# Performance work log

Measured on AMD Instinct MI355X. Metric: run time of the kernel, lower is better.

The kernel has to match this reference:

```python
import jax, jax.numpy as jnp
import numpy as np

B = 16384       # batch size
P = 2           # fixed pooling factor per bag (offsets are arange * P)
NTAB = 26       # number of sparse feature tables
NROWS = 100000  # rows per embedding table
D = 128         # embedding dim == ln_bot[-1]
LN_BOT = [13, 512, 256, 128]
LN_TOP = [479, 1024, 512, 256, 1]


def setup_inputs() -> dict:
    key = jax.random.key(0)
    ks = jax.random.split(key, 32)
    inp = {}
    inp['dense_x'] = jax.random.normal(ks[0], (B, LN_BOT[0]), dtype=jnp.float32)
    # offsets: uniform stride-P bags (EmbeddingBag offsets)
    inp['lS_o'] = jnp.broadcast_to(jnp.arange(B, dtype=jnp.int64) * P, (NTAB, B))
    inp['lS_i'] = jax.random.randint(ks[1], (NTAB, B * P), 0, NROWS, dtype=jnp.int64)
    # embedding tables, uniform(-sqrt(1/n), sqrt(1/n))
    bound = float(np.sqrt(1.0 / NROWS))
    inp['emb_tables'] = jax.random.uniform(ks[2], (NTAB, NROWS, D), dtype=jnp.float32,
                                           minval=-bound, maxval=bound)
    # bot MLP params (He-style scaled normal)
    ki = 3
    for i in range(len(LN_BOT) - 1):
        n, m = LN_BOT[i], LN_BOT[i + 1]
        inp[f'bw{i}'] = jax.random.normal(ks[ki], (m, n), dtype=jnp.float32) * np.sqrt(2.0 / (m + n)); ki += 1
        inp[f'bb{i}'] = jax.random.normal(ks[ki], (m,), dtype=jnp.float32) * np.sqrt(1.0 / m); ki += 1
    for i in range(len(LN_TOP) - 1):
        n, m = LN_TOP[i], LN_TOP[i + 1]
        inp[f'tw{i}'] = jax.random.normal(ks[ki], (m, n), dtype=jnp.float32) * np.sqrt(2.0 / (m + n)); ki += 1
        inp[f'tb{i}'] = jax.random.normal(ks[ki], (m,), dtype=jnp.float32) * np.sqrt(1.0 / m); ki += 1
    return inp


def _mlp(x, Ws, bs, sigmoid_layer):
    for i, (W, b) in enumerate(zip(Ws, bs)):
        x = x @ W.T + b
        x = jax.nn.sigmoid(x) if i == sigmoid_layer else jax.nn.relu(x)
    return x


def reference(dense_x, lS_o, lS_i, emb_tables,
              bw0, bb0, bw1, bb1, bw2, bb2,
              tw0, tb0, tw1, tb1, tw2, tb2, tw3, tb3):
    # bot MLP (sigmoid_bot = -1 -> all ReLU)
    x = _mlp(dense_x, [bw0, bw1, bw2], [bb0, bb1, bb2], sigmoid_layer=-1)  # [B, D]

    # multi-table EmbeddingBag sum pooling. Offsets (lS_o) are uniform stride-P
    # arange bags, so sum pooling is a gather + reshape + sum over P.
    def pool_one(table, idx):
        return table[idx].reshape(B, P, D).sum(axis=1)  # [B, D]
    ly = jax.vmap(pool_one)(emb_tables, lS_i)  # [NTAB, B, D]

    # dot interaction (arch_interaction_itself=False -> strict lower triangle)
    T = jnp.concatenate([x[:, None, :], jnp.transpose(ly, (1, 0, 2))], axis=1)  # [B, 27, D]
    Z = jnp.einsum('bid,bjd->bij', T, T)  # [B, 27, 27]
    ni = NTAB + 1
    li, lj = jnp.tril_indices(ni, k=-1)
    Zflat = Z[:, li, lj]  # [B, 351]
    R = jnp.concatenate([x, Zflat], axis=1)  # [B, 479]

    # top MLP (sigmoid at last layer, sigmoid_top = 3)
    p = _mlp(R, [tw0, tw1, tw2, tw3], [tb0, tb1, tb2, tb3], sigmoid_layer=3)
    return p  # [B, 1]
```

## Files before the change

### kernel.cpp

```cpp
#include <hip/hip_runtime.h>
#include <hip/hip_bf16.h>
#include <math.h>

#define BATCH 16384
#define NTAB 26
#define DIM 128
#define NROWS 100000

typedef short bf16x8 __attribute__((ext_vector_type(8)));
typedef float f32x4 __attribute__((ext_vector_type(4)));
typedef float f32x16 __attribute__((ext_vector_type(16)));

__device__ __forceinline__ ushort f2b(float f) {
  union { float f; unsigned u; } c; c.f = f;
  unsigned r = (c.u + 0x7fffu + ((c.u >> 16) & 1u)) >> 16;
  return (ushort)r;
}
__device__ __forceinline__ float b2f(ushort u) {
  union { unsigned u; float f; } c; c.u = (unsigned)u << 16;
  return c.f;
}

__device__ __forceinline__ void gload_lds16(const void* g, void* l) {
  __builtin_amdgcn_global_load_lds(
      (const __attribute__((address_space(1))) void*)g,
      (__attribute__((address_space(3))) void*)l, 16, 0, 0);
}

__global__ __launch_bounds__(256) void cvt_all_kernel(
    const float* __restrict__ bw1, const float* __restrict__ bw2,
    const float* __restrict__ tw0, const float* __restrict__ tw1,
    const float* __restrict__ tw2,
    ushort* __restrict__ o1, ushort* __restrict__ o2, ushort* __restrict__ o3,
    ushort* __restrict__ o4, ushort* __restrict__ o5) {
  int i = blockIdx.x * 256 + threadIdx.x;
  switch (blockIdx.y) {
    case 0: if (i < 256 * 512) o1[i] = f2b(bw1[i]); break;
    case 1: if (i < 128 * 256) o2[i] = f2b(bw2[i]); break;
    case 2: if (i < 1024 * 512) {
      int r = i >> 9, c = i & 511;
      o3[i] = (c < 479) ? f2b(tw0[(size_t)r * 479 + c]) : (ushort)0;
    } break;
    case 3: if (i < 512 * 1024) o4[i] = f2b(tw1[i]); break;
    case 4: if (i < 256 * 512) o5[i] = f2b(tw2[i]); break;
  }
}

__global__ __launch_bounds__(256) void bot0_kernel(const float* __restrict__ x,
    const float* __restrict__ W, const float* __restrict__ bias, ushort* __restrict__ y) {
  int b = blockIdx.x >> 1;
  int m = ((blockIdx.x & 1) << 8) | threadIdx.x;
  const float* xr = x + (size_t)b * 13;
  const float* wr = W + (size_t)m * 13;
  float acc = bias[m];
#pragma unroll
  for (int k = 0; k < 13; k++) acc = fmaf(xr[k], wr[k], acc);
  y[(size_t)b * 512 + m] = f2b(fmaxf(acc, 0.f));
}

__global__ __launch_bounds__(256) void embint_kernel(
    const float* __restrict__ tables, const int* __restrict__ lS_i,
    const ushort* __restrict__ xb, ushort* __restrict__ R) {
  __shared__ ushort Tls[4][32 * 128];
  const int wave = threadIdx.x >> 6, lane = threadIdx.x & 63;
  const int b = blockIdx.x * 4 + wave;
  char* tl = (char*)Tls[wave];

  *(uint*)(tl + lane * 4) = *(const uint*)(xb + (size_t)b * 128 + lane * 2);
#pragma unroll
  for (int r = 27; r < 32; r++)
    *(uint*)(tl + r * 256 + ((lane * 4) ^ ((r & 7) << 4))) = 0;
#pragma unroll 4
  for (int t = 0; t < NTAB; t++) {
    const int* idx = lS_i + ((size_t)t << 15) + (b << 1);
    int i0 = idx[0], i1 = idx[1];
    float2 v0 = ((const float2*)(tables + ((size_t)t * NROWS + i0) * DIM))[lane];
    float2 v1 = ((const float2*)(tables + ((size_t)t * NROWS + i1) * DIM))[lane];
    ushort2 s; s.x = f2b(v0.x + v1.x); s.y = f2b(v0.y + v1.y);
    int row = t + 1;
    *(uint*)(tl + row * 256 + ((lane * 4) ^ ((row & 7) << 4))) = *(uint*)&s;
  }
  __syncthreads();

  const int row = lane & 31;
  const int khb = (lane >> 5) * 16;
  const int swz = (row & 7) << 4;
  f32x16 z = {};
#pragma unroll
  for (int ks = 0; ks < 8; ks++) {
    bf16x8 a = *(const bf16x8*)(tl + row * 256 + ((ks * 32 + khb) ^ swz));
    z = __builtin_amdgcn_mfma_f32_32x32x16_bf16(a, a, z, 0, 0, 0);
  }

  ushort* Rb = R + (size_t)b * 512;
  *(uint*)(Rb + lane * 2) = *(const uint*)(tl + lane * 4);
  if (lane < 33) Rb[479 + lane] = 0;
  const int j = lane & 31;
  const int rb4 = (lane >> 5) * 4;
#pragma unroll
  for (int r = 0; r < 16; r++) {
    int i = (r & 3) + 8 * (r >> 2) + rb4;
    if (i <= 26 && j < i) Rb[DIM + (i * (i - 1)) / 2 + j] = f2b(z[r]);
  }
}

#define SLOT_BYTES 49152
template <int ACT>
__global__ __launch_bounds__(512, 2) void gemm256_kernel(
    const ushort* __restrict__ A, const ushort* __restrict__ W,
    const float* __restrict__ bias, ushort* __restrict__ C, int K, int ldc) {
  __shared__ char lds[3 * SLOT_BYTES];
  const int tid = threadIdx.x;
  const int lane = tid & 63, wid = tid >> 6;
  const int wm = wid >> 2, wn = wid & 3;

  const int nwg = gridDim.x * gridDim.y;
  const int orig = blockIdx.y * gridDim.x + blockIdx.x;
  const int q = nwg >> 3, r8 = nwg & 7;
  const int xcd = orig & 7, pos = orig >> 3;
  const int swzid = (xcd < r8 ? xcd * (q + 1) : r8 * (q + 1) + (xcd - r8) * q) + pos;
  const int m0 = (swzid / gridDim.x) * 256, n0 = (swzid % gridDim.x) * 128;
  const int NK = K >> 6;

  const int srow = tid >> 3;
  const int scolb = (tid & 7) << 4;

#pragma unroll
  for (int kt = 0; kt < 2; kt++) {
    char* As = lds + kt * SLOT_BYTES;
    char* Bs = As + 32768;
    const int k0 = kt * 64;
#pragma unroll
    for (int i = 0; i < 4; i++) {
      int row = i * 64 + srow;
      int colb = scolb ^ ((row & 7) << 4);
      gload_lds16(A + (size_t)(m0 + row) * K + k0 + (colb >> 1), As + i * 8192 + wid * 1024);
    }
#pragma unroll
    for (int i = 0; i < 2; i++) {
      int row = i * 64 + srow;
      int colb = scolb ^ ((row & 7) << 4);
      gload_lds16(W + (size_t)(n0 + row) * K + k0 + (colb >> 1), Bs + i * 8192 + wid * 1024);
    }
  }

  f32x4 acc[8][2] = {};
  const int fr = lane & 15;
  const int fkb = (lane >> 4) * 16;

  for (int kt = 0; kt < NK; kt++) {
    if (kt + 1 < NK) { asm volatile("s_waitcnt vmcnt(6)" ::: "memory"); }
    else             { asm volatile("s_waitcnt vmcnt(0)" ::: "memory"); }
    __builtin_amdgcn_sched_barrier(0);
    __builtin_amdgcn_s_barrier();
    __builtin_amdgcn_sched_barrier(0);

    const char* As = lds + (kt % 3) * SLOT_BYTES;
    const char* Bs = As + 32768;
    char* Ad = lds + ((kt + 2) % 3) * SLOT_BYTES;
    char* Bd = Ad + 32768;
    const int k2 = (kt + 2) * 64;
    const bool do_stage = (kt + 2 < NK);

#pragma unroll
    for (int kh = 0; kh < 2; kh++) {
      bf16x8 a[8], b[2];
#pragma unroll
      for (int mf = 0; mf < 8; mf++) {
        int row = wm * 128 + mf * 16 + fr;
        int colb = (kh * 64 + fkb) ^ ((row & 7) << 4);
        a[mf] = *(const bf16x8*)(As + row * 128 + colb);
      }
#pragma unroll
      for (int nf = 0; nf < 2; nf++) {
        int row = wn * 32 + nf * 16 + fr;
        int colb = (kh * 64 + fkb) ^ ((row & 7) << 4);
        b[nf] = *(const bf16x8*)(Bs + row * 128 + colb);
      }
      if (do_stage) {
#pragma unroll
        for (int i = kh * 2; i < kh * 2 + 2; i++) {
          int row = i * 64 + srow;
          int colb = scolb ^ ((row & 7) << 4);
          gload_lds16(A + (size_t)(m0 + row) * K + k2 + (colb >> 1), Ad + i * 8192 + wid * 1024);
        }
        {
          int row = kh * 64 + srow;
          int colb = scolb ^ ((row & 7) << 4);
          gload_lds16(W + (size_t)(n0 + row) * K + k2 + (colb >> 1), Bd + kh * 8192 + wid * 1024);
        }
      }
      __builtin_amdgcn_sched_barrier(0);
      __builtin_amdgcn_s_barrier();
      asm volatile("s_waitcnt lgkmcnt(0)" ::: "memory");
      __builtin_amdgcn_sched_barrier(0);
      __builtin_amdgcn_s_setprio(1);
#pragma unroll
      for (int mf = 0; mf < 8; mf++)
#pragma unroll
        for (int nf = 0; nf < 2; nf++)
          acc[mf][nf] = __builtin_amdgcn_mfma_f32_16x16x32_bf16(a[mf], b[nf], acc[mf][nf], 0, 0, 0);
      __builtin_amdgcn_s_setprio(0);
      if (kh == 0) {
        __builtin_amdgcn_sched_barrier(0);
        __builtin_amdgcn_s_barrier();
        __builtin_amdgcn_sched_barrier(0);
      }
    }
  }

  const int cr = lane & 15, rh = (lane >> 4) * 4;
#pragma unroll
  for (int nf = 0; nf < 2; nf++) {
    int n = n0 + wn * 32 + nf * 16 + cr;
    float bs = bias[n];
#pragma unroll
    for (int mf = 0; mf < 8; mf++) {
      int mb = m0 + wm * 128 + mf * 16 + rh;
#pragma unroll
      for (int r = 0; r < 4; r++) {
        float v = acc[mf][nf][r] + bs;
        if (ACT) v = fmaxf(v, 0.f);
        C[(size_t)(mb + r) * ldc + n] = f2b(v);
      }
    }
  }
}

template <int ACT>
__global__ __launch_bounds__(256) void gemm_bf16_kernel(
    const ushort* __restrict__ A, const ushort* __restrict__ W,
    const float* __restrict__ bias, ushort* __restrict__ C, int K, int ldc) {
  __shared__ ushort As[128 * 32];
  __shared__ ushort Bs[128 * 32];
  const int tid = threadIdx.x;
  const int lane = tid & 63, wave = tid >> 6;
  const int m0 = blockIdx.y * 128, n0 = blockIdx.x * 128;
  const int wr = wave >> 1, wc = wave & 1;

  const int srow = lane >> 2;
  const int skp = (lane & 3) * 8;
  const ushort* Ag = A + (size_t)(m0 + wave * 16 + srow) * K + skp;
  const ushort* Wg = W + (size_t)(n0 + wave * 16 + srow) * K + skp;
  ushort* AsW = &As[(wave * 16) * 32];
  ushort* BsW = &Bs[(wave * 16) * 32];

  f32x4 acc[4][4] = {};
  const int fr = lane & 15;
  const int fk = (lane >> 4) * 8;

  for (int k0 = 0; k0 < K; k0 += 32) {
    gload_lds16(Ag + k0, AsW);
    gload_lds16(Ag + (size_t)64 * K + k0, AsW + 64 * 32);
    gload_lds16(Wg + k0, BsW);
    gload_lds16(Wg + (size_t)64 * K + k0, BsW + 64 * 32);
    __syncthreads();
    bf16x8 a[4], b[4];
#pragma unroll
    for (int i = 0; i < 4; i++) {
      a[i] = *(const bf16x8*)&As[(wr * 64 + i * 16 + fr) * 32 + fk];
      b[i] = *(const bf16x8*)&Bs[(wc * 64 + i * 16 + fr) * 32 + fk];
    }
#pragma unroll
    for (int i = 0; i < 4; i++)
#pragma unroll
      for (int j = 0; j < 4; j++)
        acc[i][j] = __builtin_amdgcn_mfma_f32_16x16x32_bf16(a[i], b[j], acc[i][j], 0, 0, 0);
    __syncthreads();
  }

  const int col_l = lane & 15, row_h = (lane >> 4) * 4;
#pragma unroll
  for (int j = 0; j < 4; j++) {
    int n = n0 + wc * 64 + j * 16 + col_l;
    float bs = bias[n];
#pragma unroll
    for (int i = 0; i < 4; i++) {
      int mbase = m0 + wr * 64 + i * 16 + row_h;
#pragma unroll
      for (int r = 0; r < 4; r++) {
        float v = acc[i][j][r] + bs;
        if (ACT) v = fmaxf(v, 0.f);
        C[(size_t)(mbase + r) * ldc + n] = f2b(v);
      }
    }
  }
}

__global__ __launch_bounds__(256) void final_kernel(const ushort* __restrict__ A,
    const float* __restrict__ w, const float* __restrict__ bias, float* __restrict__ out) {
  int row = blockIdx.x * 4 + (threadIdx.x >> 6);
  int lane = threadIdx.x & 63;
  ushort4 a4 = ((const ushort4*)(A + (size_t)row * 256))[lane];
  float4 wv = ((const float4*)w)[lane];
  float s = b2f(a4.x) * wv.x + b2f(a4.y) * wv.y + b2f(a4.z) * wv.z + b2f(a4.w) * wv.w;
#pragma unroll
  for (int off = 32; off >= 1; off >>= 1) s += __shfl_xor(s, off);
  if (lane == 0) out[row] = 1.f / (1.f + expf(-(s + bias[0])));
}

extern "C" void kernel_launch(void* const* d_in, const int* in_sizes, int n_in,
                              void* d_out, int out_size, void* d_ws, size_t ws_size,
                              hipStream_t stream) {
  const float* dense_x = (const float*)d_in[0];
  const int* lS_i = (const int*)d_in[2];
  const float* emb = (const float*)d_in[3];
  const float* bw0 = (const float*)d_in[4];
  const float* bb0 = (const float*)d_in[5];
  const float* bw1 = (const float*)d_in[6];
  const float* bb1 = (const float*)d_in[7];
  const float* bw2 = (const float*)d_in[8];
  const float* bb2 = (const float*)d_in[9];
  const float* tw0 = (const float*)d_in[10];
  const float* tb0 = (const float*)d_in[11];
  const float* tw1 = (const float*)d_in[12];
  const float* tb1 = (const float*)d_in[13];
  const float* tw2 = (const float*)d_in[14];
  const float* tb2 = (const float*)d_in[15];
  const float* tw3 = (const float*)d_in[16];
  const float* tb3 = (const float*)d_in[17];
  float* out = (float*)d_out;

  char* w = (char*)d_ws;
  ushort* xb  = (ushort*)w; w += (size_t)BATCH * 128 * 2;
  ushort* x1  = (ushort*)w; w += (size_t)BATCH * 512 * 2;
  ushort* x2  = (ushort*)w; w += (size_t)BATCH * 256 * 2;
  ushort* R   = (ushort*)w; w += (size_t)BATCH * 512 * 2;
  ushort* t1  = (ushort*)w; w += (size_t)BATCH * 1024 * 2;
  ushort* wb1 = (ushort*)w; w += 256 * 512 * 2;
  ushort* wb2 = (ushort*)w; w += 128 * 256 * 2;
  ushort* wt0 = (ushort*)w; w += 1024 * 512 * 2;
  ushort* wt1 = (ushort*)w; w += 512 * 1024 * 2;
  ushort* wt2 = (ushort*)w; w += 256 * 512 * 2;
  ushort* t2 = x1;
  ushort* t3 = x2;

  cvt_all_kernel<<<dim3(2048, 5), 256, 0, stream>>>(bw1, bw2, tw0, tw1, tw2,
                                                    wb1, wb2, wt0, wt1, wt2);

  bot0_kernel<<<BATCH * 2, 256, 0, stream>>>(dense_x, bw0, bb0, x1);
  gemm_bf16_kernel<1><<<dim3(2, BATCH / 128), 256, 0, stream>>>(x1, wb1, bb1, x2, 512, 256);
  gemm_bf16_kernel<1><<<dim3(1, BATCH / 128), 256, 0, stream>>>(x2, wb2, bb2, xb, 256, 128);

  embint_kernel<<<BATCH / 4, 256, 0, stream>>>(emb, lS_i, xb, R);

  gemm256_kernel<1><<<dim3(1024 / 128, BATCH / 256), 512, 0, stream>>>(R,  wt0, tb0, t1, 512, 1024);
  gemm256_kernel<1><<<dim3(512 / 128,  BATCH / 256), 512, 0, stream>>>(t1, wt1, tb1, t2, 1024, 512);
  gemm_bf16_kernel<1><<<dim3(2, BATCH / 128), 256, 0, stream>>>(t2, wt2, tb2, t3, 512, 256);
  final_kernel<<<BATCH / 4, 256, 0, stream>>>(t3, tw3, tb3, out);
}
```

Measured before the change: 222.8 us.

## Fuse weight conversion with bottom layer and last GEMM with final dot, swizzle LDS

Merges the weight-conversion and first bottom-MLP kernels into one launch, and fuses the 512→256 top GEMM with the final 256→1 sigmoid layer so the intermediate stays in LDS instead of going through global memory. It also XOR-swizzles the LDS layout in the generic bf16 GEMM to reduce bank conflicts, and raises the unroll on the embedding gather loop. The fused tail kernel uses 64-row tiles covering all 256 output columns, which changes occupancy and tiling for that stage.

```diff
diff --git a/kernel.cpp b/kernel.cpp
--- a/kernel.cpp
+++ b/kernel.cpp
@@ -27,35 +27,39 @@
       (__attribute__((address_space(3))) void*)l, 16, 0, 0);
 }
 
-__global__ __launch_bounds__(256) void cvt_all_kernel(
+__global__ __launch_bounds__(256) void prep_kernel(
+    const float* __restrict__ x, const float* __restrict__ W0,
+    const float* __restrict__ b0, ushort* __restrict__ y,
     const float* __restrict__ bw1, const float* __restrict__ bw2,
     const float* __restrict__ tw0, const float* __restrict__ tw1,
     const float* __restrict__ tw2,
     ushort* __restrict__ o1, ushort* __restrict__ o2, ushort* __restrict__ o3,
     ushort* __restrict__ o4, ushort* __restrict__ o5) {
-  int i = blockIdx.x * 256 + threadIdx.x;
-  switch (blockIdx.y) {
+  int blk = blockIdx.x;
+  if (blk < 2 * BATCH) {
+    int b = blk >> 1;
+    int m = ((blk & 1) << 8) | threadIdx.x;
+    const float* xr = x + (size_t)b * 13;
+    const float* wr = W0 + (size_t)m * 13;
+    float acc = b0[m];
+#pragma unroll
+    for (int k = 0; k < 13; k++) acc = fmaf(xr[k], wr[k], acc);
+    y[(size_t)b * 512 + m] = f2b(fmaxf(acc, 0.f));
+    return;
+  }
+  int cb = blk - 2 * BATCH;
+  int c = cb >> 11;
+  int i = (cb & 2047) * 256 + threadIdx.x;
+  switch (c) {
     case 0: if (i < 256 * 512) o1[i] = f2b(bw1[i]); break;
     case 1: if (i < 128 * 256) o2[i] = f2b(bw2[i]); break;
     case 2: if (i < 1024 * 512) {
-      int r = i >> 9, c = i & 511;
-      o3[i] = (c < 479) ? f2b(tw0[(size_t)r * 479 + c]) : (ushort)0;
+      int r = i >> 9, cc = i & 511;
+      o3[i] = (cc < 479) ? f2b(tw0[(size_t)r * 479 + cc]) : (ushort)0;
     } break;
     case 3: if (i < 512 * 1024) o4[i] = f2b(tw1[i]); break;
     case 4: if (i < 256 * 512) o5[i] = f2b(tw2[i]); break;
   }
-}
-
-__global__ __launch_bounds__(256) void bot0_kernel(const float* __restrict__ x,
-    const float* __restrict__ W, const float* __restrict__ bias, ushort* __restrict__ y) {
-  int b = blockIdx.x >> 1;
-  int m = ((blockIdx.x & 1) << 8) | threadIdx.x;
-  const float* xr = x + (size_t)b * 13;
-  const float* wr = W + (size_t)m * 13;
-  float acc = bias[m];
-#pragma unroll
-  for (int k = 0; k < 13; k++) acc = fmaf(xr[k], wr[k], acc);
-  y[(size_t)b * 512 + m] = f2b(fmaxf(acc, 0.f));
 }
 
 __global__ __launch_bounds__(256) void embint_kernel(
@@ -70,7 +74,7 @@
 #pragma unroll
   for (int r = 27; r < 32; r++)
     *(uint*)(tl + r * 256 + ((lane * 4) ^ ((r & 7) << 4))) = 0;
-#pragma unroll 4
+#pragma unroll 8
   for (int t = 0; t < NTAB; t++) {
     const int* idx = lS_i + ((size_t)t << 15) + (b << 1);
     int i0 = idx[0], i1 = idx[1];
@@ -239,15 +243,16 @@
   const int wr = wave >> 1, wc = wave & 1;
 
   const int srow = lane >> 2;
-  const int skp = (lane & 3) * 8;
-  const ushort* Ag = A + (size_t)(m0 + wave * 16 + srow) * K + skp;
-  const ushort* Wg = W + (size_t)(n0 + wave * 16 + srow) * K + skp;
+  const int scolb = ((lane & 3) << 4) ^ ((srow & 3) << 4);
+  const ushort* Ag = A + (size_t)(m0 + wave * 16 + srow) * K + (scolb >> 1);
+  const ushort* Wg = W + (size_t)(n0 + wave * 16 + srow) * K + (scolb >> 1);
   ushort* AsW = &As[(wave * 16) * 32];
   ushort* BsW = &Bs[(wave * 16) * 32];
 
   f32x4 acc[4][4] = {};
   const int fr = lane & 15;
-  const int fk = (lane >> 4) * 8;
+  const int fkb = (lane >> 4) * 16;
+  const int fswz = (fr & 3) << 4;
 
   for (int k0 = 0; k0 < K; k0 += 32) {
     gload_lds16(Ag + k0, AsW);
@@ -258,8 +263,8 @@
     bf16x8 a[4], b[4];
 #pragma unroll
     for (int i = 0; i < 4; i++) {
-      a[i] = *(const bf16x8*)&As[(wr * 64 + i * 16 + fr) * 32 + fk];
-      b[i] = *(const bf16x8*)&Bs[(wc * 64 + i * 16 + fr) * 32 + fk];
+      a[i] = *(const bf16x8*)((const char*)As + (wr * 64 + i * 16 + fr) * 64 + (fkb ^ fswz));
+      b[i] = *(const bf16x8*)((const char*)Bs + (wc * 64 + i * 16 + fr) * 64 + (fkb ^ fswz));
     }
 #pragma unroll
     for (int i = 0; i < 4; i++)
@@ -287,16 +292,73 @@
   }
 }
 
-__global__ __launch_bounds__(256) void final_kernel(const ushort* __restrict__ A,
-    const float* __restrict__ w, const float* __restrict__ bias, float* __restrict__ out) {
-  int row = blockIdx.x * 4 + (threadIdx.x >> 6);
-  int lane = threadIdx.x & 63;
-  ushort4 a4 = ((const ushort4*)(A + (size_t)row * 256))[lane];
-  float4 wv = ((const float4*)w)[lane];
-  float s = b2f(a4.x) * wv.x + b2f(a4.y) * wv.y + b2f(a4.z) * wv.z + b2f(a4.w) * wv.w;
-#pragma unroll
-  for (int off = 32; off >= 1; off >>= 1) s += __shfl_xor(s, off);
-  if (lane == 0) out[row] = 1.f / (1.f + expf(-(s + bias[0])));
+__global__ __launch_bounds__(256) void t2final_kernel(
+    const ushort* __restrict__ A, const ushort* __restrict__ W,
+    const float* __restrict__ bias, const float* __restrict__ w3,
+    const float* __restrict__ b3, float* __restrict__ out) {
+  __shared__ char smem[64 * 264 * 2];
+  ushort* As = (ushort*)smem;
+  ushort* Bs = (ushort*)(smem + 4096);
+  ushort* Ct = (ushort*)smem;
+  const int tid = threadIdx.x;
+  const int lane = tid & 63, wave = tid >> 6;
+  const int m0 = blockIdx.x * 64;
+
+  const int srow = lane >> 2;
+  const int scolb = ((lane & 3) << 4) ^ ((srow & 3) << 4);
+  const ushort* Ag = A + (size_t)(m0 + wave * 16 + srow) * 512 + (scolb >> 1);
+  const ushort* Wg = W + (size_t)(wave * 16 + srow) * 512 + (scolb >> 1);
+
+  f32x4 acc[4][4] = {};
+  const int fr = lane & 15;
+  const int fkb = (lane >> 4) * 16;
+  const int fswz = (fr & 3) << 4;
+
+  for (int k0 = 0; k0 < 512; k0 += 32) {
+    gload_lds16(Ag + k0, (char*)As + wave * 1024);
+#pragma unroll
+    for (int i = 0; i < 4; i++)
+      gload_lds16(Wg + (size_t)(i * 64) * 512 + k0, (char*)Bs + i * 4096 + wave * 1024);
+    __syncthreads();
+    bf16x8 a[4], b[4];
+#pragma unroll
+    for (int i = 0; i < 4; i++) {
+      a[i] = *(const bf16x8*)((const char*)As + (i * 16 + fr) * 64 + (fkb ^ fswz));
+      b[i] = *(const bf16x8*)((const char*)Bs + (wave * 64 + i * 16 + fr) * 64 + (fkb ^ fswz));
+    }
+#pragma unroll
+    for (int i = 0; i < 4; i++)
+#pragma unroll
+      for (int j = 0; j < 4; j++)
+        acc[i][j] = __builtin_amdgcn_mfma_f32_16x16x32_bf16(a[i], b[j], acc[i][j], 0, 0, 0);
+    __syncthreads();
+  }
+
+  const int col_l = lane & 15, row_h = (lane >> 4) * 4;
+#pragma unroll
+  for (int j = 0; j < 4; j++) {
+    int n = wave * 64 + j * 16 + col_l;
+    float bs = bias[n];
+#pragma unroll
+    for (int i = 0; i < 4; i++) {
+      int mb = i * 16 + row_h;
+#pragma unroll
+      for (int r = 0; r < 4; r++)
+        Ct[(size_t)(mb + r) * 264 + n] = f2b(fmaxf(acc[i][j][r] + bs, 0.f));
+    }
+  }
+  __syncthreads();
+
+  const float4 wv = ((const float4*)w3)[lane];
+  const float bf = b3[0];
+  for (int rr = 0; rr < 16; rr++) {
+    int row = wave * 16 + rr;
+    ushort4 a4 = *(const ushort4*)&Ct[(size_t)row * 264 + lane * 4];
+    float s = b2f(a4.x) * wv.x + b2f(a4.y) * wv.y + b2f(a4.z) * wv.z + b2f(a4.w) * wv.w;
+#pragma unroll
+    for (int off = 32; off >= 1; off >>= 1) s += __shfl_xor(s, off);
+    if (lane == 0) out[m0 + row] = 1.f / (1.f + expf(-(s + bf)));
+  }
 }
 
 extern "C" void kernel_launch(void* const* d_in, const int* in_sizes, int n_in,
@@ -333,12 +395,10 @@
   ushort* wt1 = (ushort*)w; w += 512 * 1024 * 2;
   ushort* wt2 = (ushort*)w; w += 256 * 512 * 2;
   ushort* t2 = x1;
-  ushort* t3 = x2;
-
-  cvt_all_kernel<<<dim3(2048, 5), 256, 0, stream>>>(bw1, bw2, tw0, tw1, tw2,
-                                                    wb1, wb2, wt0, wt1, wt2);
-
-  bot0_kernel<<<BATCH * 2, 256, 0, stream>>>(dense_x, bw0, bb0, x1);
+
+  prep_kernel<<<2 * BATCH + 5 * 2048, 256, 0, stream>>>(
+      dense_x, bw0, bb0, x1, bw1, bw2, tw0, tw1, tw2, wb1, wb2, wt0, wt1, wt2);
+
   gemm_bf16_kernel<1><<<dim3(2, BATCH / 128), 256, 0, stream>>>(x1, wb1, bb1, x2, 512, 256);
   gemm_bf16_kernel<1><<<dim3(1, BATCH / 128), 256, 0, stream>>>(x2, wb2, bb2, xb, 256, 128);
 
@@ -346,6 +406,5 @@
 
   gemm256_kernel<1><<<dim3(1024 / 128, BATCH / 256), 512, 0, stream>>>(R,  wt0, tb0, t1, 512, 1024);
   gemm256_kernel<1><<<dim3(512 / 128,  BATCH / 256), 512, 0, stream>>>(t1, wt1, tb1, t2, 1024, 512);
-  gemm_bf16_kernel<1><<<dim3(2, BATCH / 128), 256, 0, stream>>>(t2, wt2, tb2, t3, 512, 256);
-  final_kernel<<<BATCH / 4, 256, 0, stream>>>(t3, tw3, tb3, out);
-}
+  t2final_kernel<<<BATCH / 64, 256, 0, stream>>>(t2, wt2, tb2, tw3, tb3, out);
+}
```

Result: faster. 218.1 us (median of 2 runs) (-2.1%).
